# Kernel tuning notes

Hardware: AMD Instinct MI355X
Metric: run time of the kernel (lower is better)

The kernel has to match this reference:

```python
import jax, jax.numpy as jnp
import numpy as np

MAX_DISP = 4          # displacement radius -> 9x9 = 81 output channels
B, C, H, W = 8, 128, 96, 160


def setup_inputs() -> dict:
    key = jax.random.key(0)
    k1, k2 = jax.random.split(key)
    tensorFirst = jax.random.normal(k1, (B, C, H, W), dtype=jnp.float32)
    tensorSecond = jax.random.normal(k2, (B, C, H, W), dtype=jnp.float32)
    return {"tensorFirst": tensorFirst, "tensorSecond": tensorSecond}


def correlation(first, second):
    # first, second: [B, C, H, W]
    b, c, h, w = first.shape
    d = MAX_DISP
    pad = jnp.pad(second, ((0, 0), (0, 0), (d, d), (d, d)))  # [B,C,H+8,W+8]
    inv_c = jnp.asarray(1.0 / c, dtype=first.dtype)
    # channel order: (dy+4)*9 + (dx+4), dx fastest (matches CUDA kernel)
    chans = [
        (first * pad[:, :, dy:dy + h, dx:dx + w]).sum(axis=1) * inv_c
        for dy in range(2 * d + 1)
        for dx in range(2 * d + 1)
    ]
    return jnp.stack(chans, axis=1)  # [B, 81, H, W]


def reference(tensorFirst, tensorSecond):
    return correlation(tensorFirst, tensorSecond)
```

## Files before the change

### kernel.cpp

```cpp
#include <hip/hip_runtime.h>
#include <stdint.h>


typedef __attribute__((ext_vector_type(8))) short bf16x8;
typedef __attribute__((ext_vector_type(4))) float f32x4;

constexpr int Bn = 8, Cn = 128, Hn = 96, Wn = 160;
constexpr int CHS = Hn * Wn;
constexpr int YP  = Hn + 8;
constexpr int XPD = Wn + 16;
constexpr size_t SECP_OCTS  = (size_t)Bn * 16 * YP * XPD;
constexpr size_t SECP_BYTES = SECP_OCTS * 16;

__device__ __forceinline__ uint32_t bf16rne(float f) {
    uint32_t u = __float_as_uint(f);
    return (u + 0x7FFFu + ((u >> 16) & 1u)) >> 16;
}
__device__ __forceinline__ uint32_t pk(float a, float b) {
    return bf16rne(a) | (bf16rne(b) << 16);
}

__global__ __launch_bounds__(256)
void prepass(const float* __restrict__ sec, uint4* __restrict__ secp)
{
    const int idx = blockIdx.x * 256 + threadIdx.x;
    const int xp  = idx % XPD;
    const int t1  = idx / XPD;
    const int yp  = t1 % YP;
    const int t2  = t1 / YP;
    const int oc  = t2 & 15;
    const int b   = t2 >> 4;
    const int y = yp - 4, x = xp - 8;
    uint4 o = make_uint4(0u, 0u, 0u, 0u);
    if (y >= 0 && y < Hn && x >= 0 && x < Wn) {
        const float* src = sec + ((size_t)b * Cn + 8 * oc) * CHS + (size_t)y * Wn + x;
        float f[8];
        #pragma unroll
        for (int j = 0; j < 8; ++j) f[j] = src[(size_t)j * CHS];
        o.x = pk(f[0], f[1]); o.y = pk(f[2], f[3]);
        o.z = pk(f[4], f[5]); o.w = pk(f[6], f[7]);
    }
    secp[idx] = o;
}

__global__ __launch_bounds__(512, 4)
void corrmain(const float* __restrict__ first, const uint4* __restrict__ secp,
              float* __restrict__ out)
{
    __shared__ __align__(16) char smemRaw[62464];
    uint4* smemS = (uint4*)smemRaw;
    float* smE   = (float*)smemRaw;

    const int tid  = threadIdx.x;
    const int w    = tid >> 6;
    const int lane = tid & 63;
    const int quad = lane >> 4;
    const int n16  = lane & 15;
    const int s    = w & 1;
    const int rp   = w >> 1;

    const int d    = (int)blockIdx.x + 10 * ((int)blockIdx.y + 12 * (int)blockIdx.z);
    const int tile = (d & 7) * 120 + (d >> 3);
    const int b    = tile / 120;
    const int rem  = tile % 120;
    const int y0   = (rem / 10) * 8;
    const int x0   = (rem % 10) * 16;

    size_t gsl[3];
    #pragma unroll
    for (int i = 0; i < 3; ++i) {
        int sig = i * 512 + tid;
        int q   = sig / 384;
        int rm  = sig % 384;
        int row = rm / 24;
        int xw  = rm % 24;
        gsl[i] = ((size_t)(b * 16 + q) * YP + (y0 + row)) * XPD + (x0 + 4 + xw);
    }
    const size_t kstep = (size_t)4 * YP * XPD;

    #pragma unroll
    for (int i = 0; i < 3; ++i)
        __builtin_amdgcn_global_load_lds(
            (const uint32_t*)(secp + gsl[i]),
            (uint32_t*)(smemS + i * 512 + w * 64),
            16, 0, 0);

    bf16x8 aF[4];
    {
        const float* fp = first + (size_t)b * Cn * CHS
                        + (size_t)(y0 + 2 * rp + (n16 >> 3)) * Wn
                        + x0 + 8 * s + (n16 & 7);
        float fA[4][8];
        #pragma unroll
        for (int kc = 0; kc < 4; ++kc)
            #pragma unroll
            for (int j = 0; j < 8; ++j)
                fA[kc][j] = fp[(size_t)(32 * kc + 8 * quad + j) * CHS];
        #pragma unroll
        for (int kc = 0; kc < 4; ++kc) {
            union { uint32_t u[4]; bf16x8 v; } cv;
            cv.u[0] = pk(fA[kc][0], fA[kc][1]); cv.u[1] = pk(fA[kc][2], fA[kc][3]);
            cv.u[2] = pk(fA[kc][4], fA[kc][5]); cv.u[3] = pk(fA[kc][6], fA[kc][7]);
            aF[kc] = cv.v;
        }
    }

    f32x4 acc[10];
    #pragma unroll
    for (int zi = 0; zi < 10; ++zi) acc[zi] = (f32x4){0.f, 0.f, 0.f, 0.f};

    __syncthreads();

    #pragma unroll
    for (int kc = 0; kc < 4; ++kc) {
        if (kc < 3) {
            const int nb = (kc + 1) & 1;
            #pragma unroll
            for (int i = 0; i < 3; ++i)
                __builtin_amdgcn_global_load_lds(
                    (const uint32_t*)(secp + gsl[i] + kstep * (kc + 1)),
                    (uint32_t*)(smemS + nb * 1536 + i * 512 + w * 64),
                    16, 0, 0);
        }
        const int cb = (kc & 1) * 1536;
        #pragma unroll
        for (int zi = 0; zi < 10; ++zi) {
            union { uint4 u; bf16x8 v; } bf;
            bf.u = smemS[cb + quad * 384 + (2 * rp + zi) * 24 + 8 * s + n16];
            acc[zi] = __builtin_amdgcn_mfma_f32_16x16x32_bf16(
                          aF[kc], bf.v, acc[zi], 0, 0, 0);
        }
        __syncthreads();
    }

    const float inv = 1.0f / 128.0f;
    const int wb = w * 1952;
    #pragma unroll
    for (int zi = 0; zi < 10; ++zi)
        #pragma unroll
        for (int reg = 0; reg < 4; ++reg) {
            const int rh  = quad >> 1;
            const int px  = (quad & 1) * 4 + reg;
            const int dyc = zi - rh;
            const int dxc = n16 - px;
            if (dyc >= 0 && dyc <= 8 && dxc >= 0 && dxc <= 8)
                smE[wb + ((rh * 81) + dyc * 9 + dxc) * 12 + px] = acc[zi][reg] * inv;
        }
    __syncthreads();
    float* ob = out + (size_t)b * 81 * CHS + (size_t)(y0 + 2 * rp) * Wn + x0 + 8 * s;
    #pragma unroll
    for (int ii = 0; ii < 6; ++ii) {
        int slot = lane + ii * 64;
        if (slot < 324) {
            int rh  = (slot >= 162) ? 1 : 0;
            int rm2 = slot - 162 * rh;
            int c   = rm2 >> 1, g = rm2 & 1;
            float4 v = *(const float4*)&smE[wb + (rh * 81 + c) * 12 + 4 * g];
            *(float4*)(ob + (size_t)c * CHS + (size_t)rh * Wn + 4 * g) = v;
        }
    }
}

__global__ __launch_bounds__(512, 4)
void corrfb(const float* __restrict__ first, const float* __restrict__ second,
            float* __restrict__ out)
{
    __shared__ uint4 smem[16 * 32 * 4];

    const int tid  = threadIdx.x;
    const int w    = tid >> 6;
    const int lane = tid & 63;
    const int quad = lane >> 4;
    const int n16  = lane & 15;
    const int r    = w;

    const int d    = (int)blockIdx.x + 10 * ((int)blockIdx.y + 12 * (int)blockIdx.z);
    const int tile = (d & 7) * 120 + (d >> 3);
    const int b    = tile / 120;
    const int rem  = tile % 120;
    const int y0   = (rem / 10) * 8;
    const int x0   = (rem % 10) * 16;
    const int y    = y0 + r;

    const float* sb = second + (size_t)b * Cn * CHS;
    int goff[4], lpos[4];
    bool val[4];
    #pragma unroll
    for (int i = 0; i < 4; ++i) {
        int e   = tid + i * 512;
        int row = e >> 7;
        int xw  = (e >> 2) & 31;
        int q   = e & 3;
        int gy  = y0 + row - 4, gx = x0 + xw - 8;
        val[i]  = (gy >= 0) && (gy < Hn) && (gx >= 0) && (gx < Wn);
        goff[i] = val[i] ? (8 * q * CHS + gy * Wn + gx) : 0;
        lpos[i] = (row * 32 + xw) * 4 + ((q + xw + (xw >> 2)) & 3);
    }

    int bo[2];
    #pragma unroll
    for (int t = 0; t < 2; ++t) {
        int xwr = 16 * t + n16;
        bo[t] = xwr * 4 + ((quad + xwr + (xwr >> 2)) & 3);
    }

    const float* fp = first + (size_t)b * Cn * CHS + (size_t)y * Wn + x0 + n16;

    f32x4 acc[9][2];
    #pragma unroll
    for (int dy = 0; dy < 9; ++dy)
        #pragma unroll
        for (int t = 0; t < 2; ++t)
            acc[dy][t] = (f32x4){0.f, 0.f, 0.f, 0.f};

    float f0[2][8];
    #pragma unroll
    for (int i = 0; i < 2; ++i)
        #pragma unroll
        for (int j = 0; j < 8; ++j)
            f0[i][j] = sb[goff[i] + (size_t)j * CHS];

    #pragma unroll
    for (int kc = 0; kc < 4; ++kc) {
        #pragma unroll
        for (int i = 0; i < 2; ++i) {
            uint4 o;
            o.x = pk(f0[i][0], f0[i][1]); o.y = pk(f0[i][2], f0[i][3]);
            o.z = pk(f0[i][4], f0[i][5]); o.w = pk(f0[i][6], f0[i][7]);
            if (!val[i]) o = make_uint4(0u, 0u, 0u, 0u);
            smem[lpos[i]] = o;
        }
        float f1[2][8], fa[8];
        #pragma unroll
        for (int i = 0; i < 2; ++i)
            #pragma unroll
            for (int j = 0; j < 8; ++j)
                f1[i][j] = sb[goff[2 + i] + (size_t)(32 * kc + j) * CHS];
        #pragma unroll
        for (int j = 0; j < 8; ++j)
            fa[j] = fp[(size_t)(32 * kc + 8 * quad + j) * CHS];
        #pragma unroll
        for (int i = 0; i < 2; ++i) {
            uint4 o;
            o.x = pk(f1[i][0], f1[i][1]); o.y = pk(f1[i][2], f1[i][3]);
            o.z = pk(f1[i][4], f1[i][5]); o.w = pk(f1[i][6], f1[i][7]);
            if (!val[2 + i]) o = make_uint4(0u, 0u, 0u, 0u);
            smem[lpos[2 + i]] = o;
        }
        bf16x8 aF;
        {
            union { uint32_t u[4]; bf16x8 v; } cv;
            cv.u[0] = pk(fa[0], fa[1]); cv.u[1] = pk(fa[2], fa[3]);
            cv.u[2] = pk(fa[4], fa[5]); cv.u[3] = pk(fa[6], fa[7]);
            aF = cv.v;
        }
        __syncthreads();
        if (kc < 3) {
            #pragma unroll
            for (int i = 0; i < 2; ++i)
                #pragma unroll
                for (int j = 0; j < 8; ++j)
                    f0[i][j] = sb[goff[i] + (size_t)(32 * (kc + 1) + j) * CHS];
        }
        #pragma unroll
        for (int dy = 0; dy < 9; ++dy) {
            const int rb = (r + dy) * 128;
            #pragma unroll
            for (int t = 0; t < 2; ++t) {
                union { uint4 u; bf16x8 v; } bf;
                bf.u = smem[rb + bo[t]];
                acc[dy][t] = __builtin_amdgcn_mfma_f32_16x16x32_bf16(
                                 aF, bf.v, acc[dy][t], 0, 0, 0);
            }
        }
        __syncthreads();
    }

    const float inv = 1.0f / 128.0f;
    float* sm = (float*)smem;
    float* ob = out + (size_t)b * 81 * CHS + (size_t)y * Wn + x0;
    const int wb = w * 540;
    #pragma unroll
    for (int ck = 0; ck < 3; ++ck) {
        #pragma unroll
        for (int dd = 0; dd < 3; ++dd)
            #pragma unroll
            for (int t = 0; t < 2; ++t)
                #pragma unroll
                for (int reg = 0; reg < 4; ++reg) {
                    int mm  = quad * 4 + reg;
                    int dxc = 16 * t + n16 - mm - 4;
                    if (dxc >= 0 && dxc <= 8)
                        sm[wb + (dd * 9 + dxc) * 20 + mm] = acc[ck * 3 + dd][t][reg] * inv;
                }
        __syncthreads();
        #pragma unroll
        for (int ii = 0; ii < 2; ++ii) {
            int slot = lane + ii * 64;
            if (slot < 108) {
                int chn = slot >> 2, g = slot & 3;
                float4 v = *(const float4*)&sm[wb + chn * 20 + 4 * g];
                int ch = (ck * 3 + chn / 9) * 9 + chn % 9;
                *(float4*)(ob + (size_t)ch * CHS + 4 * g) = v;
            }
        }
        __syncthreads();
    }
}

extern "C" void kernel_launch(void* const* d_in, const int* in_sizes, int n_in,
                              void* d_out, int out_size, void* d_ws, size_t ws_size,
                              hipStream_t stream) {
    (void)in_sizes; (void)n_in; (void)out_size;
    const float* first  = (const float*)d_in[0];
    const float* second = (const float*)d_in[1];
    float* out = (float*)d_out;

    if (ws_size >= SECP_BYTES) {
        uint4* secp = (uint4*)d_ws;
        prepass<<<dim3((unsigned)(SECP_OCTS / 256), 1, 1), dim3(256, 1, 1), 0, stream>>>(
            second, secp);
        corrmain<<<dim3(10, 12, 8), dim3(512, 1, 1), 0, stream>>>(first, secp, out);
    } else {
        corrfb<<<dim3(Wn / 16, Hn / 8, Bn), dim3(512, 1, 1), 0, stream>>>(
            first, second, out);
    }
}
```

Measured before the change: 177.7 us.

## Load all channel chunks into LDS at once and drop double buffering

Replaces the 4-stage double-buffered LDS pipeline for the packed second tensor with one bulk load of all 16 channel octets into a 96 KB shared buffer. The MFMA loop then runs with a single barrier instead of one per chunk. The first-tensor global loads are now issued before the LDS loads, and the barrier between the per-wave epilogue write and read is removed, since each wave uses only its own region. In exchange, shared memory per block grows a lot and the launch bound drops to 2 blocks, which cuts occupancy and loses the overlap of loading with compute.

```diff
diff --git a/kernel.cpp b/kernel.cpp
--- a/kernel.cpp
+++ b/kernel.cpp
@@ -43,11 +43,11 @@
     secp[idx] = o;
 }
 
-__global__ __launch_bounds__(512, 4)
+__global__ __launch_bounds__(512, 2)
 void corrmain(const float* __restrict__ first, const uint4* __restrict__ secp,
               float* __restrict__ out)
 {
-    __shared__ __align__(16) char smemRaw[62464];
+    __shared__ __align__(16) char smemRaw[98304];
     uint4* smemS = (uint4*)smemRaw;
     float* smE   = (float*)smemRaw;
 
@@ -66,43 +66,37 @@
     const int y0   = (rem / 10) * 8;
     const int x0   = (rem % 10) * 16;
 
-    size_t gsl[3];
-    #pragma unroll
-    for (int i = 0; i < 3; ++i) {
-        int sig = i * 512 + tid;
-        int q   = sig / 384;
-        int rm  = sig % 384;
-        int row = rm / 24;
-        int xw  = rm % 24;
-        gsl[i] = ((size_t)(b * 16 + q) * YP + (y0 + row)) * XPD + (x0 + 4 + xw);
-    }
-    const size_t kstep = (size_t)4 * YP * XPD;
-
-    #pragma unroll
-    for (int i = 0; i < 3; ++i)
+    const float* fp = first + (size_t)b * Cn * CHS
+                    + (size_t)(y0 + 2 * rp + (n16 >> 3)) * Wn
+                    + x0 + 8 * s + (n16 & 7);
+    float fA[4][8];
+    #pragma unroll
+    for (int kc = 0; kc < 4; ++kc)
+        #pragma unroll
+        for (int j = 0; j < 8; ++j)
+            fA[kc][j] = fp[(size_t)(32 * kc + 8 * quad + j) * CHS];
+
+    #pragma unroll
+    for (int i = 0; i < 12; ++i) {
+        const int sig = i * 512 + tid;
+        const int oc  = sig / 384;
+        const int rm  = sig % 384;
+        const int row = rm / 24;
+        const int xw  = rm % 24;
+        const int goff = ((b * 16 + oc) * YP + (y0 + row)) * XPD + (x0 + 4 + xw);
         __builtin_amdgcn_global_load_lds(
-            (const uint32_t*)(secp + gsl[i]),
+            (const uint32_t*)(secp + goff),
             (uint32_t*)(smemS + i * 512 + w * 64),
             16, 0, 0);
+    }
 
     bf16x8 aF[4];
-    {
-        const float* fp = first + (size_t)b * Cn * CHS
-                        + (size_t)(y0 + 2 * rp + (n16 >> 3)) * Wn
-                        + x0 + 8 * s + (n16 & 7);
-        float fA[4][8];
-        #pragma unroll
-        for (int kc = 0; kc < 4; ++kc)
-            #pragma unroll
-            for (int j = 0; j < 8; ++j)
-                fA[kc][j] = fp[(size_t)(32 * kc + 8 * quad + j) * CHS];
-        #pragma unroll
-        for (int kc = 0; kc < 4; ++kc) {
-            union { uint32_t u[4]; bf16x8 v; } cv;
-            cv.u[0] = pk(fA[kc][0], fA[kc][1]); cv.u[1] = pk(fA[kc][2], fA[kc][3]);
-            cv.u[2] = pk(fA[kc][4], fA[kc][5]); cv.u[3] = pk(fA[kc][6], fA[kc][7]);
-            aF[kc] = cv.v;
-        }
+    #pragma unroll
+    for (int kc = 0; kc < 4; ++kc) {
+        union { uint32_t u[4]; bf16x8 v; } cv;
+        cv.u[0] = pk(fA[kc][0], fA[kc][1]); cv.u[1] = pk(fA[kc][2], fA[kc][3]);
+        cv.u[2] = pk(fA[kc][4], fA[kc][5]); cv.u[3] = pk(fA[kc][6], fA[kc][7]);
+        aF[kc] = cv.v;
     }
 
     f32x4 acc[10];
@@ -113,25 +107,16 @@
 
     #pragma unroll
     for (int kc = 0; kc < 4; ++kc) {
-        if (kc < 3) {
-            const int nb = (kc + 1) & 1;
-            #pragma unroll
-            for (int i = 0; i < 3; ++i)
-                __builtin_amdgcn_global_load_lds(
-                    (const uint32_t*)(secp + gsl[i] + kstep * (kc + 1)),
-                    (uint32_t*)(smemS + nb * 1536 + i * 512 + w * 64),
-                    16, 0, 0);
-        }
-        const int cb = (kc & 1) * 1536;
         #pragma unroll
         for (int zi = 0; zi < 10; ++zi) {
             union { uint4 u; bf16x8 v; } bf;
-            bf.u = smemS[cb + quad * 384 + (2 * rp + zi) * 24 + 8 * s + n16];
+            bf.u = smemS[(4 * kc + quad) * 384 + (2 * rp + zi) * 24 + 8 * s + n16];
             acc[zi] = __builtin_amdgcn_mfma_f32_16x16x32_bf16(
                           aF[kc], bf.v, acc[zi], 0, 0, 0);
         }
-        __syncthreads();
-    }
+    }
+
+    __syncthreads();
 
     const float inv = 1.0f / 128.0f;
     const int wb = w * 1952;
@@ -146,7 +131,6 @@
             if (dyc >= 0 && dyc <= 8 && dxc >= 0 && dxc <= 8)
                 smE[wb + ((rh * 81) + dyc * 9 + dxc) * 12 + px] = acc[zi][reg] * inv;
         }
-    __syncthreads();
     float* ob = out + (size_t)b * 81 * CHS + (size_t)(y0 + 2 * rp) * Wn + x0 + 8 * s;
     #pragma unroll
     for (int ii = 0; ii < 6; ++ii) {
```

New measurement: 185.8 us. 4.6% more time.
